# Performance work log

Hardware: AMD Instinct MI355X
Metric: run time of the kernel (lower is better)

## Reference

```python
import jax, jax.numpy as jnp
import numpy as np

B = 4096          # batch; ALSO the QLSTM sequence length (forward unbinds dim 0)
IN_DIM = 8
HIDDEN = 16       # hidden_dim == n_qubits (required for torch broadcast to work)
TAGSET = 10

_H = jnp.array([[1, 1], [1, -1]], jnp.complex64) * (2.0 ** -0.5)

# ---- single/two-qubit gate builders (qiskit conventions) ----

def _rz(t):
    t = jnp.asarray(t, jnp.float32)
    em = jnp.exp(-0.5j * t)
    ep = jnp.exp(0.5j * t)
    z = jnp.zeros((), jnp.complex64)
    return jnp.stack([jnp.stack([em, z]), jnp.stack([z, ep])])

def _ry(t):
    t = jnp.asarray(t, jnp.float32)
    c = jnp.cos(0.5 * t).astype(jnp.complex64)
    s = jnp.sin(0.5 * t).astype(jnp.complex64)
    return jnp.stack([jnp.stack([c, -s]), jnp.stack([s, c])])

def _phase(lam):  # qiskit p / u1 gate: diag(1, e^{i*lam})
    lam = jnp.asarray(lam, jnp.float32)
    one = jnp.ones((), jnp.complex64)
    z = jnp.zeros((), jnp.complex64)
    return jnp.stack([jnp.stack([one, z]), jnp.stack([z, jnp.exp(1j * lam)])])

# ---- statevector primitives: state has shape (2,)*n, axis i == qubit i ----

def _apply1(state, gate, w):
    s = jnp.tensordot(gate, state, axes=([1], [w]))
    return jnp.moveaxis(s, 0, w)

def _cnot(state, c, t):
    s = jnp.moveaxis(state, (c, t), (0, 1))
    s = jnp.stack([s[0], s[1][::-1]], axis=0)  # flip target where control==1
    return jnp.moveaxis(s, (0, 1), (c, t))

def _expZ(state, w):
    p = state.real ** 2 + state.imag ** 2
    p = jnp.moveaxis(p, w, 0).reshape(2, -1).sum(axis=1)
    return p[0] - p[1]

def _conv(state, a, b, p):
    state = _apply1(state, _rz(-np.pi / 2), b)
    state = _cnot(state, b, a)
    state = _apply1(state, _rz(p[0]), a)
    state = _apply1(state, _ry(p[1]), b)
    state = _cnot(state, a, b)
    state = _apply1(state, _ry(p[2]), b)
    state = _cnot(state, b, a)
    state = _apply1(state, _rz(np.pi / 2), a)
    return state

def _pool(state, a, b, p):
    state = _apply1(state, _rz(-np.pi / 2), b)
    state = _cnot(state, b, a)
    state = _apply1(state, _rz(p[0]), a)
    state = _apply1(state, _ry(p[1]), b)
    state = _cnot(state, a, b)
    state = _apply1(state, _ry(p[2]), b)
    return state

def _qcnn_one(x, c1, p1, c2, p2, c3, p3):
    state = jnp.zeros((2,) * 8, jnp.complex64).at[(0,) * 8].set(1.0)
    for _ in range(2):  # ZFeatureMap(8), reps=2: H layer + P(2*x_i)
        for q in range(8):
            state = _apply1(state, _H, q)
        for q in range(8):
            state = _apply1(state, _phase(2.0 * x[q]), q)
    for k, i in enumerate(range(0, 8, 2)):   # c1 on pairs (0,1)(2,3)(4,5)(6,7)
        state = _conv(state, i, i + 1, c1[k])
    for k in range(4):                        # p1 on (0,4)(1,5)(2,6)(3,7)
        state = _pool(state, k, k + 4, p1[k])
    for k, i in enumerate(range(0, 4, 2)):   # c2 on (0,1)(2,3)
        state = _conv(state, i, i + 1, c2[k])
    for k in range(2):                        # p2 on (0,2)(1,3)
        state = _pool(state, k, k + 2, p2[k])
    state = _conv(state, 0, 1, c3[0])
    state = _pool(state, 0, 1, p3[0])
    return _expZ(state, 7)  # observable 'Z'+'I'*7 == Z on qubit 7

def _sampler_one(x, w):
    state = jnp.zeros((2, 2), jnp.complex64).at[0, 0].set(1.0)
    state = _apply1(state, _ry(x[0]), 0)
    state = _apply1(state, _ry(x[1]), 1)
    state = _cnot(state, 0, 1)
    state = _apply1(state, _ry(w[0]), 0)
    state = _apply1(state, _ry(w[1]), 1)
    state = _cnot(state, 0, 1)
    state = _apply1(state, _ry(w[2]), 0)
    state = _apply1(state, _ry(w[3]), 1)
    probs = state.real ** 2 + state.imag ** 2  # [q0, q1]
    return probs.T.reshape(4)  # qiskit little-endian: index = 2*q1 + q0

# ---- QLSTM QLayer, exact closed form ----
# product state RX(v_i + theta_i)|0>, CNOT ring (0,1)..(n-2,n-1),(n-1,0), <Z_j>:
#   <Z_0> = prod_{k>=1} cos(phi_k);  <Z_j> = prod_{k<=j} cos(phi_k) for j>=1.

def _qlayer(v, theta):  # v: [1, n]
    c = jnp.cos(v + theta)
    head = jnp.prod(c[:, 1:], axis=1, keepdims=True)
    rest = jnp.cumprod(c, axis=1)[:, 1:]
    return jnp.concatenate([head, rest], axis=1)

def _forward(inputs, c1, p1, c2, p2, c3, p3, w_smp, Wf, bf, Wi, bi, Wu, bu, Wo, bo, th_f, th_i, th_u, th_o, Wt, bt):
    qcnn = jax.vmap(lambda x: _qcnn_one(x, c1, p1, c2, p2, c3, p3))(inputs)[:, None]  # [B,1]
    samp = jax.vmap(lambda x: _sampler_one(x, w_smp))(inputs)  # [B,4]
    seq = inputs[:, None, :]  # [T=B, 1, 8] -- unsqueeze(1) then unbind(dim=0)

    def step(carry, x):
        hx, cx = carry
        comb = jnp.concatenate([x, hx], axis=1)  # [1, 24]
        f = jax.nn.sigmoid(_qlayer(comb @ Wf.T + bf, th_f))
        i = jax.nn.sigmoid(_qlayer(comb @ Wi.T + bi, th_i))
        g = jnp.tanh(_qlayer(comb @ Wu.T + bu, th_u))
        o = jax.nn.sigmoid(_qlayer(comb @ Wo.T + bo, th_o))
        cx = f * cx + i * g
        hx = o * jnp.tanh(cx)
        return (hx, cx), hx

    z0 = jnp.zeros((1, HIDDEN), jnp.float32)
    _, outs = jax.lax.scan(step, (z0, z0), seq)  # [B, 1, 16]
    tag = jax.nn.log_softmax(outs @ Wt.T + bt, axis=-1)  # [B, 1, 10]
    return qcnn, tag, samp

def setup_inputs() -> dict:
    key = jax.random.key(0)
    ks = jax.random.split(key, 32)
    pi = float(np.pi)
    u = lambda k, s: jax.random.uniform(k, s, jnp.float32, -pi, pi)
    fan = IN_DIM + HIDDEN
    lw = lambda k: jax.random.normal(k, (HIDDEN, fan), jnp.float32) * fan ** -0.5
    lb = lambda k: jax.random.normal(k, (HIDDEN,), jnp.float32) * fan ** -0.5
    return {
        "inputs": jax.random.normal(ks[0], (B, IN_DIM), jnp.float32),
        "c1": u(ks[1], (4, 3)), "p1": u(ks[2], (4, 3)),
        "c2": u(ks[3], (2, 3)), "p2": u(ks[4], (2, 3)),
        "c3": u(ks[5], (1, 3)), "p3": u(ks[6], (1, 3)),
        "w_smp": u(ks[7], (4,)),
        "Wf": lw(ks[8]), "bf": lb(ks[9]),
        "Wi": lw(ks[10]), "bi": lb(ks[11]),
        "Wu": lw(ks[12]), "bu": lb(ks[13]),
        "Wo": lw(ks[14]), "bo": lb(ks[15]),
        "th_f": u(ks[16], (HIDDEN,)), "th_i": u(ks[17], (HIDDEN,)),
        "th_u": u(ks[18], (HIDDEN,)), "th_o": u(ks[19], (HIDDEN,)),
        "Wt": jax.random.normal(ks[20], (TAGSET, HIDDEN), jnp.float32) * HIDDEN ** -0.5,
        "bt": jax.random.normal(ks[21], (TAGSET,), jnp.float32) * HIDDEN ** -0.5,
    }

def reference(inputs, c1, p1, c2, p2, c3, p3, w_smp, Wf, bf, Wi, bi, Wu, bu, Wo, bo, th_f, th_i, th_u, th_o, Wt, bt):
    return _forward(inputs, c1, p1, c2, p2, c3, p3, w_smp, Wf, bf, Wi, bi, Wu, bu, Wo, bo, th_f, th_i, th_u, th_o, Wt, bt)
```

## Files before the change

### kernel.cpp

```cpp
#include <hip/hip_runtime.h>
#include <math.h>


typedef unsigned int uint32x2 __attribute__((ext_vector_type(2)));

#define INV2PI 0.15915494309189535f
#define NCHUNK 128
#define CHUNK  32
#define WARM   96
#define MAXSTEP (CHUNK + WARM)

__device__ __forceinline__ float2 cmulf(float2 a, float2 b){
  return make_float2(a.x*b.x - a.y*b.y, a.x*b.y + a.y*b.x);
}
template<int CTRL>
__device__ __forceinline__ float dpp_mov(float v){
  return __int_as_float(__builtin_amdgcn_update_dpp(
      0, __float_as_int(v), CTRL, 0xF, 0xF, false));
}

#define PFX_LEVEL(p, CTRLSTR) \
  asm("v_mul_f32_dpp %0, %0, %0 " CTRLSTR " row_mask:0xf bank_mask:0xf" : "+v"(p))
#define FMAC_DPP(acc, src, w, CTRLSTR) \
  asm("v_fmac_f32_dpp %0, %1, %2 " CTRLSTR " row_mask:0xf bank_mask:0xf" \
      : "+v"(acc) : "v"(src), "v"(w))

struct SerState {
  float wh[16];
  float esc, gA, gB;
  int   e;
  bool  c32, c16, b0, b1, mQ;
};

__device__ __forceinline__ void lstm_step(const SerState& S, float ax,
                                          float& cx, float& h){
  const float r0  = h;
  const float r4  = dpp_mov<0x124>(r0);
  const float r8  = dpp_mov<0x128>(r0);
  const float r12 = dpp_mov<0x12C>(r0);
  float a0 = fmaf(S.wh[0],  r0,  ax);
  float a1 = S.wh[4]  * r4;
  float a2 = S.wh[8]  * r8;
  float a3 = S.wh[12] * r12;
  FMAC_DPP(a0, r0,  S.wh[1],  "row_ror:1");
  FMAC_DPP(a1, r4,  S.wh[5],  "row_ror:1");
  FMAC_DPP(a2, r8,  S.wh[9],  "row_ror:1");
  FMAC_DPP(a3, r12, S.wh[13], "row_ror:1");
  FMAC_DPP(a0, r0,  S.wh[2],  "row_ror:2");
  FMAC_DPP(a1, r4,  S.wh[6],  "row_ror:2");
  FMAC_DPP(a2, r8,  S.wh[10], "row_ror:2");
  FMAC_DPP(a3, r12, S.wh[14], "row_ror:2");
  FMAC_DPP(a0, r0,  S.wh[3],  "row_ror:3");
  FMAC_DPP(a1, r4,  S.wh[7],  "row_ror:3");
  FMAC_DPP(a2, r8,  S.wh[11], "row_ror:3");
  FMAC_DPP(a3, r12, S.wh[15], "row_ror:3");
  const float acc = (a0+a1) + (a2+a3);

  const float c = __builtin_amdgcn_cosf(acc);
  float p = c;
  float sfx = (S.e==0) ? 1.0f : c;
  PFX_LEVEL(p,   "row_shr:1");
  PFX_LEVEL(sfx, "row_shl:1");
  PFX_LEVEL(p,   "row_shr:2");
  PFX_LEVEL(sfx, "row_shl:2");
  PFX_LEVEL(p,   "row_shr:4");
  PFX_LEVEL(sfx, "row_shl:4");
  PFX_LEVEL(p,   "row_shr:8");
  PFX_LEVEL(sfx, "row_shl:8");
  const float v = (S.e==0) ? sfx : p;

  const float ex  = __builtin_amdgcn_exp2f(v * S.esc);
  const float sg  = __builtin_amdgcn_rcpf(1.0f + ex);
  const float act = fmaf(S.gA, sg, S.gB);

  const unsigned au = __float_as_uint(act);
  uint32x2 r32 = __builtin_amdgcn_permlane32_swap(au, au, false, false);
  const unsigned o32u = S.c32 ? r32[0] : r32[1];
  uint32x2 rA = __builtin_amdgcn_permlane16_swap(au, au, false, false);
  const unsigned oAu = S.c16 ? rA[0] : rA[1];
  uint32x2 rB = __builtin_amdgcn_permlane16_swap(o32u, o32u, false, false);
  const unsigned oBu = S.c16 ? rB[0] : rB[1];
  const float fau = __uint_as_float(au);
  const float fA  = __uint_as_float(oAu);
  const float f32 = __uint_as_float(o32u);
  const float fB  = __uint_as_float(oBu);
  const float pLoA = S.b0 ? fA  : fau;
  const float pHiA = S.b0 ? fB  : f32;
  const float act0 = S.b1 ? pHiA : pLoA;
  const float pLoB = S.b0 ? fau : fA;
  const float pHiB = S.b0 ? f32 : fB;
  const float act3 = S.b1 ? pLoB : pHiB;
  const float Q    = S.mQ ? fA*f32 : fau*fB;

  cx = fmaf(act0, cx, Q);
  const float em = __builtin_amdgcn_exp2f(cx * -2.885390082f);
  const float rr = __builtin_amdgcn_rcpf(1.0f + em);
  h = fmaf(act3+act3, rr, -act3);
}

__device__ __forceinline__ void ser_init(SerState& S, int lane,
    const float* Wf, const float* Wi, const float* Wu, const float* Wo){
  const int g = lane >> 4, e = lane & 15;
  S.e = e;
  const float* W = (g==0)?Wf:(g==1)?Wi:(g==2)?Wu:Wo;
  int probe = __builtin_amdgcn_update_dpp(0, e, 0x121, 0xF, 0xF, false);
  const int sgn = (probe == ((e+1)&15)) ? 1 : -1;
  #pragma unroll
  for (int d=0; d<16; d++)
    S.wh[d] = W[e*24 + 8 + ((e + sgn*d + 32) & 15)] * INV2PI;
  S.esc = (g==2) ? -2.885390082f : -1.442695041f;
  S.gA  = (g==2) ? 2.0f : 1.0f;
  S.gB  = (g==2) ? -1.0f : 0.0f;
  uint32x2 p32 = __builtin_amdgcn_permlane32_swap((unsigned)lane,(unsigned)lane,false,false);
  S.c32 = (p32[0] == (unsigned)(lane ^ 32));
  uint32x2 p16 = __builtin_amdgcn_permlane16_swap((unsigned)lane,(unsigned)lane,false,false);
  S.c16 = (p16[0] == (unsigned)(lane ^ 16));
  S.b0 = (g & 1) != 0;
  S.b1 = (g & 2) != 0;
  S.mQ = (g==0) || (g==3);
}

__device__ __forceinline__ void apply_diag(float2 (&s)[4], int q, float2 d0, float2 d1){
  const int lane = threadIdx.x & 63;
  #pragma unroll
  for (int r=0;r<4;r++){
    int bit = (q>=6) ? ((r >> (7-q)) & 1) : ((lane >> (5-q)) & 1);
    s[r] = cmulf(s[r], bit ? d1 : d0);
  }
}
__device__ __forceinline__ void apply_real(float2 (&s)[4], int q,
                                           float m00, float m01, float m10, float m11){
  const int lane = threadIdx.x & 63;
  if (q >= 6){
    const int st = 1 << (7-q);
    for (int base=0;base<4;base++){
      if (base & st) continue;
      float2 a = s[base], b2 = s[base+st];
      s[base]    = make_float2(fmaf(m00,a.x, m01*b2.x), fmaf(m00,a.y, m01*b2.y));
      s[base+st] = make_float2(fmaf(m10,a.x, m11*b2.x), fmaf(m10,a.y, m11*b2.y));
    }
  } else {
    const int mask = 1 << (5-q);
    const bool hi = (lane & mask) != 0;
    #pragma unroll
    for (int r=0;r<4;r++){
      float ox = __shfl_xor(s[r].x, mask);
      float oy = __shfl_xor(s[r].y, mask);
      float2 m = s[r];
      if (!hi) s[r] = make_float2(fmaf(m00,m.x, m01*ox), fmaf(m00,m.y, m01*oy));
      else     s[r] = make_float2(fmaf(m10,ox, m11*m.x), fmaf(m10,oy, m11*m.y));
    }
  }
}
__device__ __forceinline__ void cnot_g(float2 (&s)[4], int c, int t){
  const int lane = threadIdx.x & 63;
  if (t >= 6){
    const int st = 1 << (7-t);
    for (int base=0;base<4;base++){
      if (base & st) continue;
      int cb = (c>=6) ? ((base >> (7-c)) & 1) : ((lane >> (5-c)) & 1);
      if (cb){ float2 tmp=s[base]; s[base]=s[base+st]; s[base+st]=tmp; }
    }
  } else {
    const int mask = 1 << (5-t);
    #pragma unroll
    for (int r=0;r<4;r++){
      float ox = __shfl_xor(s[r].x, mask);
      float oy = __shfl_xor(s[r].y, mask);
      int cb = (c>=6) ? ((r >> (7-c)) & 1) : ((lane >> (5-c)) & 1);
      if (cb) s[r] = make_float2(ox, oy);
    }
  }
}
__device__ void conv_g(float2 (&s)[4], int qa, int qb, const float* p){
  const float R = 0.70710678118654752f;
  apply_diag(s, qb, make_float2(R,R), make_float2(R,-R));
  cnot_g(s, qb, qa);
  float sn, cs;
  __sincosf(0.5f*p[0], &sn, &cs);
  apply_diag(s, qa, make_float2(cs,-sn), make_float2(cs,sn));
  __sincosf(0.5f*p[1], &sn, &cs);
  apply_real(s, qb, cs, -sn, sn, cs);
  cnot_g(s, qa, qb);
  __sincosf(0.5f*p[2], &sn, &cs);
  apply_real(s, qb, cs, -sn, sn, cs);
  cnot_g(s, qb, qa);
  apply_diag(s, qa, make_float2(R,-R), make_float2(R,R));
}
__device__ void pool_g(float2 (&s)[4], int qa, int qb, const float* p){
  const float R = 0.70710678118654752f;
  apply_diag(s, qb, make_float2(R,R), make_float2(R,-R));
  cnot_g(s, qb, qa);
  float sn, cs;
  __sincosf(0.5f*p[0], &sn, &cs);
  apply_diag(s, qa, make_float2(cs,-sn), make_float2(cs,sn));
  __sincosf(0.5f*p[1], &sn, &cs);
  apply_real(s, qb, cs, -sn, sn, cs);
  cnot_g(s, qa, qb);
  __sincosf(0.5f*p[2], &sn, &cs);
  apply_real(s, qb, cs, -sn, sn, cs);
}

__device__ void qcnn_body(const float* __restrict__ inputs,
                          const float* __restrict__ c1, const float* __restrict__ p1,
                          const float* __restrict__ c2, const float* __restrict__ p2,
                          const float* __restrict__ c3, const float* __restrict__ p3,
                          const float* __restrict__ w_smp,
                          float* __restrict__ out, int b, int B)
{
  const int lane = threadIdx.x & 63;
  float2 s[4];
  s[0] = make_float2(0.f,0.f); s[1]=s[0]; s[2]=s[0]; s[3]=s[0];
  if (lane == 0) s[0] = make_float2(1.f, 0.f);
  float xl[8];
  #pragma unroll
  for (int k=0;k<8;k++) xl[k] = inputs[b*8+k];
  const float R = 0.70710678118654752f;
  for (int rep=0;rep<2;rep++){
    for (int q=0;q<8;q++) apply_real(s, q, R, R, R, -R);
    for (int q=0;q<8;q++){
      float sn, cs; __sincosf(2.0f*xl[q], &sn, &cs);
      apply_diag(s, q, make_float2(1.f,0.f), make_float2(cs,sn));
    }
  }
  for (int k=0;k<4;k++) conv_g(s, 2*k, 2*k+1, c1+3*k);
  for (int k=0;k<4;k++) pool_g(s, k, k+4, p1+3*k);
  for (int k=0;k<2;k++) conv_g(s, 2*k, 2*k+1, c2+3*k);
  for (int k=0;k<2;k++) pool_g(s, k, k+2, p2+3*k);
  conv_g(s, 0, 1, c3);
  pool_g(s, 0, 1, p3);
  float v = (s[0].x*s[0].x + s[0].y*s[0].y) - (s[1].x*s[1].x + s[1].y*s[1].y)
          + (s[2].x*s[2].x + s[2].y*s[2].y) - (s[3].x*s[3].x + s[3].y*s[3].y);
  #pragma unroll
  for (int d=1; d<64; d<<=1) v += __shfl_xor(v, d);
  if (lane == 0){
    out[b] = v;
    float a00=1.f, a01=0.f, a10=0.f, a11=0.f;
    float sn, cs, t0, t1;
    #define RY0(T) { __sincosf(0.5f*(T), &sn, &cs); \
      t0 = cs*a00 - sn*a10; t1 = sn*a00 + cs*a10; a00=t0; a10=t1; \
      t0 = cs*a01 - sn*a11; t1 = sn*a01 + cs*a11; a01=t0; a11=t1; }
    #define RY1(T) { __sincosf(0.5f*(T), &sn, &cs); \
      t0 = cs*a00 - sn*a01; t1 = sn*a00 + cs*a01; a00=t0; a01=t1; \
      t0 = cs*a10 - sn*a11; t1 = sn*a10 + cs*a11; a10=t0; a11=t1; }
    #define CN01 { float tmp=a10; a10=a11; a11=tmp; }
    RY0(xl[0]); RY1(xl[1]); CN01;
    RY0(w_smp[0]); RY1(w_smp[1]); CN01;
    RY0(w_smp[2]); RY1(w_smp[3]);
    #undef RY0
    #undef RY1
    #undef CN01
    float* samp = out + B + B*10;
    samp[b*4+0] = a00*a00; samp[b*4+1] = a10*a10;
    samp[b*4+2] = a01*a01; samp[b*4+3] = a11*a11;
  }
}

extern "C" __global__ void __launch_bounds__(256)
k_all(const float* __restrict__ inputs,
      const float* __restrict__ Wf, const float* __restrict__ Wi,
      const float* __restrict__ Wu, const float* __restrict__ Wo,
      const float* __restrict__ bfv, const float* __restrict__ biv,
      const float* __restrict__ buv, const float* __restrict__ bov,
      const float* __restrict__ thf, const float* __restrict__ thi,
      const float* __restrict__ thu, const float* __restrict__ tho,
      const float* __restrict__ c1, const float* __restrict__ p1,
      const float* __restrict__ c2, const float* __restrict__ p2,
      const float* __restrict__ c3, const float* __restrict__ p3,
      const float* __restrict__ w_smp,
      const float* __restrict__ Wt, const float* __restrict__ bt,
      float* __restrict__ out, int B)
{
  __shared__ float xlds[MAXSTEP*8];
  __shared__ float hlds[16*CHUNK];

  if (blockIdx.x < NCHUNK){
    const int kc    = blockIdx.x;
    const int t_out = kc*CHUNK, t_end = t_out + CHUNK;
    const int t_start = (t_out > WARM) ? (t_out - WARM) : 0;
    const int nsteps  = t_end - t_start;

    for (int i = threadIdx.x; i < nsteps*8; i += 256)
      xlds[i] = inputs[t_start*8 + i];
    __syncthreads();

    if (threadIdx.x < 64){
      const int lane = threadIdx.x, g = lane>>4, e = lane&15;
      SerState S; ser_init(S, lane, Wf, Wi, Wu, Wo);
      const float* W  = (g==0)?Wf :(g==1)?Wi :(g==2)?Wu :Wo;
      const float* bb = (g==0)?bfv:(g==1)?biv:(g==2)?buv:bov;
      const float* th = (g==0)?thf:(g==1)?thi:(g==2)?thu:tho;
      float wx[8];
      #pragma unroll
      for (int k2=0;k2<8;k2++) wx[k2] = W[e*24+k2] * INV2PI;
      const float base = (bb[e] + th[e]) * INV2PI;

      float cx=0.f, h=0.f, hq0=0.f, hq1=0.f, hq2=0.f;
      float4 xa = *(const float4*)&xlds[0];
      float4 xb = *(const float4*)&xlds[4];
      float u0 = fmaf(wx[0],xa.x,base), u1 = wx[1]*xa.y,
            u2 = wx[2]*xa.z,            u3 = wx[3]*xa.w;
      u0 = fmaf(wx[4],xb.x,u0); u1 = fmaf(wx[5],xb.y,u1);
      u2 = fmaf(wx[6],xb.z,u2); u3 = fmaf(wx[7],xb.w,u3);
      float axc = (u0+u1)+(u2+u3);

      #pragma unroll 4
      for (int lt=0; lt<nsteps; lt++){
        const int nlt = (lt+1 < nsteps) ? (lt+1) : lt;
        const float4 na = *(const float4*)&xlds[nlt*8];
        const float4 nb = *(const float4*)&xlds[nlt*8+4];
        float v0 = fmaf(wx[0],na.x,base), v1 = wx[1]*na.y,
              v2 = wx[2]*na.z,            v3 = wx[3]*na.w;
        v0 = fmaf(wx[4],nb.x,v0); v1 = fmaf(wx[5],nb.y,v1);
        v2 = fmaf(wx[6],nb.z,v2); v3 = fmaf(wx[7],nb.w,v3);
        const float axn = (v0+v1)+(v2+v3);

        lstm_step(S, axc, cx, h);
        const int q = lt & 3;
        if      (q==0) hq0 = h;
        else if (q==1) hq1 = h;
        else if (q==2) hq2 = h;
        else {
          const int tb = t_start + lt - 3;
          if (tb >= t_out){
            const float hv = S.b1 ? (S.b0 ? h : hq2) : (S.b0 ? hq1 : hq0);
            hlds[e*CHUNK + (tb + g - t_out)] = hv;
          }
        }
        axc = axn;
      }
    }
    __syncthreads();

    if (threadIdx.x < CHUNK){
      const int s = threadIdx.x;
      float hh[16];
      #pragma unroll
      for (int e2=0;e2<16;e2++) hh[e2] = hlds[e2*CHUNK + s];
      float lg[10];
      #pragma unroll
      for (int j=0;j<10;j++){
        const float* w = Wt + j*16;
        float s0 = fmaf(w[0],hh[0], bt[j]);
        float s1 = w[1]*hh[1], s2 = w[2]*hh[2], s3 = w[3]*hh[3];
        #pragma unroll
        for (int e2=4;e2<16;e2+=4){
          s0 = fmaf(w[e2],  hh[e2],  s0);
          s1 = fmaf(w[e2+1],hh[e2+1],s1);
          s2 = fmaf(w[e2+2],hh[e2+2],s2);
          s3 = fmaf(w[e2+3],hh[e2+3],s3);
        }
        lg[j] = (s0+s1)+(s2+s3);
      }
      float m = lg[0];
      #pragma unroll
      for (int j=1;j<10;j++) m = fmaxf(m, lg[j]);
      float ss = 0.f;
      #pragma unroll
      for (int j=0;j<10;j++) ss += __expf(lg[j]-m);
      const float lse = __logf(ss) + m;
      float* tag = out + B + (size_t)(t_out + s)*10;
      #pragma unroll
      for (int j=0;j<10;j++) tag[j] = lg[j] - lse;
    }
    return;
  }

  const int b = (blockIdx.x - NCHUNK)*4 + (threadIdx.x >> 6);
  qcnn_body(inputs, c1,p1,c2,p2,c3,p3, w_smp, out, b, B);
}

extern "C" void kernel_launch(void* const* d_in, const int* in_sizes, int n_in,
                              void* d_out, int out_size, void* d_ws, size_t ws_size,
                              hipStream_t stream)
{
  const float* inputs = (const float*)d_in[0];
  const float* c1  = (const float*)d_in[1];
  const float* p1  = (const float*)d_in[2];
  const float* c2  = (const float*)d_in[3];
  const float* p2  = (const float*)d_in[4];
  const float* c3  = (const float*)d_in[5];
  const float* p3  = (const float*)d_in[6];
  const float* wsm = (const float*)d_in[7];
  const float* Wf  = (const float*)d_in[8];
  const float* bf_ = (const float*)d_in[9];
  const float* Wi  = (const float*)d_in[10];
  const float* bi_ = (const float*)d_in[11];
  const float* Wu  = (const float*)d_in[12];
  const float* bu_ = (const float*)d_in[13];
  const float* Wo  = (const float*)d_in[14];
  const float* bo_ = (const float*)d_in[15];
  const float* thf = (const float*)d_in[16];
  const float* thi = (const float*)d_in[17];
  const float* thu = (const float*)d_in[18];
  const float* tho = (const float*)d_in[19];
  const float* Wt  = (const float*)d_in[20];
  const float* bt  = (const float*)d_in[21];
  const int B = in_sizes[0] / 8;
  float* out = (float*)d_out;

  k_all<<<NCHUNK + B/4, 256, 0, stream>>>(inputs,
                                          Wf,Wi,Wu,Wo, bf_,bi_,bu_,bo_,
                                          thf,thi,thu,tho,
                                          c1,p1,c2,p2,c3,p3, wsm,
                                          Wt, bt, out, B);
}
```

Before: 133.5 us.

## Reduce QCNN to measured-qubit light cone, one thread per sample

```diff
diff --git a/kernel.cpp b/kernel.cpp
--- a/kernel.cpp
+++ b/kernel.cpp
@@ -9,6 +9,7 @@
 #define CHUNK  32
 #define WARM   96
 #define MAXSTEP (CHUNK + WARM)
+#define HLDS_LD (CHUNK + 1)
 
 __device__ __forceinline__ float2 cmulf(float2 a, float2 b){
   return make_float2(a.x*b.x - a.y*b.y, a.x*b.y + a.y*b.x);
@@ -120,140 +121,118 @@
   S.mQ = (g==0) || (g==3);
 }
 
-__device__ __forceinline__ void apply_diag(float2 (&s)[4], int q, float2 d0, float2 d1){
-  const int lane = threadIdx.x & 63;
+__device__ __forceinline__ void rz4_lo(float2 (&t)[4], float sn, float cs){
+  const float2 e0 = make_float2(cs,-sn), e1 = make_float2(cs, sn);
+  t[0]=cmulf(t[0],e0); t[1]=cmulf(t[1],e1);
+  t[2]=cmulf(t[2],e0); t[3]=cmulf(t[3],e1);
+}
+__device__ __forceinline__ void rz4_hi(float2 (&t)[4], float sn, float cs){
+  const float2 e0 = make_float2(cs,-sn), e1 = make_float2(cs, sn);
+  t[0]=cmulf(t[0],e0); t[1]=cmulf(t[1],e0);
+  t[2]=cmulf(t[2],e1); t[3]=cmulf(t[3],e1);
+}
+__device__ __forceinline__ void ry4_lo(float2 (&t)[4], float sn, float cs){
+  float2 a=t[0], b=t[1];
+  t[0]=make_float2(cs*a.x - sn*b.x, cs*a.y - sn*b.y);
+  t[1]=make_float2(sn*a.x + cs*b.x, sn*a.y + cs*b.y);
+  a=t[2]; b=t[3];
+  t[2]=make_float2(cs*a.x - sn*b.x, cs*a.y - sn*b.y);
+  t[3]=make_float2(sn*a.x + cs*b.x, sn*a.y + cs*b.y);
+}
+__device__ __forceinline__ void cnot4_loctl(float2 (&t)[4]){
+  float2 tmp=t[1]; t[1]=t[3]; t[3]=tmp;
+}
+__device__ __forceinline__ void cnot4_hictl(float2 (&t)[4]){
+  float2 tmp=t[2]; t[2]=t[3]; t[3]=tmp;
+}
+
+__device__ __forceinline__ void conv4(float2 (&t)[4], const float* p){
+  const float R = 0.70710678118654752f;
+  rz4_lo(t, -R, R);
+  cnot4_loctl(t);
+  float sn, cs;
+  __sincosf(0.5f*p[0], &sn, &cs);
+  rz4_hi(t, sn, cs);
+  __sincosf(0.5f*p[1], &sn, &cs);
+  ry4_lo(t, sn, cs);
+  cnot4_hictl(t);
+  __sincosf(0.5f*p[2], &sn, &cs);
+  ry4_lo(t, sn, cs);
+  cnot4_loctl(t);
+  rz4_hi(t, R, R);
+}
+__device__ __forceinline__ void pool4(float2 (&t)[4], const float* p){
+  const float R = 0.70710678118654752f;
+  rz4_lo(t, -R, R);
+  cnot4_loctl(t);
+  float sn, cs;
+  __sincosf(0.5f*p[0], &sn, &cs);
+  rz4_hi(t, sn, cs);
+  __sincosf(0.5f*p[1], &sn, &cs);
+  ry4_lo(t, sn, cs);
+  cnot4_hictl(t);
+  __sincosf(0.5f*p[2], &sn, &cs);
+  ry4_lo(t, sn, cs);
+}
+
+__device__ void qcnn_thread(const float* __restrict__ inputs,
+                            const float* __restrict__ c1,
+                            const float* __restrict__ p1,
+                            const float* __restrict__ w_smp,
+                            float* __restrict__ out, int b, int B)
+{
+  const float4 xa = *(const float4*)(inputs + b*8);
+  const float4 xb = *(const float4*)(inputs + b*8 + 4);
+
+  const float xs[4] = {xa.z, xa.w, xb.z, xb.w};
+  float2 v0[4], v1[4];
   #pragma unroll
-  for (int r=0;r<4;r++){
-    int bit = (q>=6) ? ((r >> (7-q)) & 1) : ((lane >> (5-q)) & 1);
-    s[r] = cmulf(s[r], bit ? d1 : d0);
+  for (int k=0;k<4;k++){
+    float sn, cs; __sincosf(2.0f*xs[k], &sn, &cs);
+    v0[k] = make_float2(0.5f*(1.0f+cs), 0.5f*sn);
+    v1[k] = make_float2(0.5f*(cs - cs*cs + sn*sn), 0.5f*(sn - 2.0f*cs*sn));
   }
-}
-__device__ __forceinline__ void apply_real(float2 (&s)[4], int q,
-                                           float m00, float m01, float m10, float m11){
-  const int lane = threadIdx.x & 63;
-  if (q >= 6){
-    const int st = 1 << (7-q);
-    for (int base=0;base<4;base++){
-      if (base & st) continue;
-      float2 a = s[base], b2 = s[base+st];
-      s[base]    = make_float2(fmaf(m00,a.x, m01*b2.x), fmaf(m00,a.y, m01*b2.y));
-      s[base+st] = make_float2(fmaf(m10,a.x, m11*b2.x), fmaf(m10,a.y, m11*b2.y));
-    }
-  } else {
-    const int mask = 1 << (5-q);
-    const bool hi = (lane & mask) != 0;
+  float2 A[4]  = {cmulf(v0[0],v0[1]), cmulf(v0[0],v1[1]),
+                  cmulf(v1[0],v0[1]), cmulf(v1[0],v1[1])};
+  float2 Bv[4] = {cmulf(v0[2],v0[3]), cmulf(v0[2],v1[3]),
+                  cmulf(v1[2],v0[3]), cmulf(v1[2],v1[3])};
+  conv4(A,  c1+3);
+  conv4(Bv, c1+9);
+
+  float ez = 0.f;
+  #pragma unroll
+  for (int i2=0;i2<2;i2++){
     #pragma unroll
-    for (int r=0;r<4;r++){
-      float ox = __shfl_xor(s[r].x, mask);
-      float oy = __shfl_xor(s[r].y, mask);
-      float2 m = s[r];
-      if (!hi) s[r] = make_float2(fmaf(m00,m.x, m01*ox), fmaf(m00,m.y, m01*oy));
-      else     s[r] = make_float2(fmaf(m10,ox, m11*m.x), fmaf(m10,oy, m11*m.y));
+    for (int i6=0;i6<2;i6++){
+      float2 t[4] = {cmulf(A[i2*2+0], Bv[i6*2+0]),
+                     cmulf(A[i2*2+0], Bv[i6*2+1]),
+                     cmulf(A[i2*2+1], Bv[i6*2+0]),
+                     cmulf(A[i2*2+1], Bv[i6*2+1])};
+      pool4(t, p1+9);
+      ez += (t[0].x*t[0].x + t[0].y*t[0].y) - (t[1].x*t[1].x + t[1].y*t[1].y)
+          + (t[2].x*t[2].x + t[2].y*t[2].y) - (t[3].x*t[3].x + t[3].y*t[3].y);
     }
   }
-}
-__device__ __forceinline__ void cnot_g(float2 (&s)[4], int c, int t){
-  const int lane = threadIdx.x & 63;
-  if (t >= 6){
-    const int st = 1 << (7-t);
-    for (int base=0;base<4;base++){
-      if (base & st) continue;
-      int cb = (c>=6) ? ((base >> (7-c)) & 1) : ((lane >> (5-c)) & 1);
-      if (cb){ float2 tmp=s[base]; s[base]=s[base+st]; s[base+st]=tmp; }
-    }
-  } else {
-    const int mask = 1 << (5-t);
-    #pragma unroll
-    for (int r=0;r<4;r++){
-      float ox = __shfl_xor(s[r].x, mask);
-      float oy = __shfl_xor(s[r].y, mask);
-      int cb = (c>=6) ? ((r >> (7-c)) & 1) : ((lane >> (5-c)) & 1);
-      if (cb) s[r] = make_float2(ox, oy);
-    }
-  }
-}
-__device__ void conv_g(float2 (&s)[4], int qa, int qb, const float* p){
-  const float R = 0.70710678118654752f;
-  apply_diag(s, qb, make_float2(R,R), make_float2(R,-R));
-  cnot_g(s, qb, qa);
-  float sn, cs;
-  __sincosf(0.5f*p[0], &sn, &cs);
-  apply_diag(s, qa, make_float2(cs,-sn), make_float2(cs,sn));
-  __sincosf(0.5f*p[1], &sn, &cs);
-  apply_real(s, qb, cs, -sn, sn, cs);
-  cnot_g(s, qa, qb);
-  __sincosf(0.5f*p[2], &sn, &cs);
-  apply_real(s, qb, cs, -sn, sn, cs);
-  cnot_g(s, qb, qa);
-  apply_diag(s, qa, make_float2(R,-R), make_float2(R,R));
-}
-__device__ void pool_g(float2 (&s)[4], int qa, int qb, const float* p){
-  const float R = 0.70710678118654752f;
-  apply_diag(s, qb, make_float2(R,R), make_float2(R,-R));
-  cnot_g(s, qb, qa);
-  float sn, cs;
-  __sincosf(0.5f*p[0], &sn, &cs);
-  apply_diag(s, qa, make_float2(cs,-sn), make_float2(cs,sn));
-  __sincosf(0.5f*p[1], &sn, &cs);
-  apply_real(s, qb, cs, -sn, sn, cs);
-  cnot_g(s, qa, qb);
-  __sincosf(0.5f*p[2], &sn, &cs);
-  apply_real(s, qb, cs, -sn, sn, cs);
-}
-
-__device__ void qcnn_body(const float* __restrict__ inputs,
-                          const float* __restrict__ c1, const float* __restrict__ p1,
-                          const float* __restrict__ c2, const float* __restrict__ p2,
-                          const float* __restrict__ c3, const float* __restrict__ p3,
-                          const float* __restrict__ w_smp,
-                          float* __restrict__ out, int b, int B)
-{
-  const int lane = threadIdx.x & 63;
-  float2 s[4];
-  s[0] = make_float2(0.f,0.f); s[1]=s[0]; s[2]=s[0]; s[3]=s[0];
-  if (lane == 0) s[0] = make_float2(1.f, 0.f);
-  float xl[8];
-  #pragma unroll
-  for (int k=0;k<8;k++) xl[k] = inputs[b*8+k];
-  const float R = 0.70710678118654752f;
-  for (int rep=0;rep<2;rep++){
-    for (int q=0;q<8;q++) apply_real(s, q, R, R, R, -R);
-    for (int q=0;q<8;q++){
-      float sn, cs; __sincosf(2.0f*xl[q], &sn, &cs);
-      apply_diag(s, q, make_float2(1.f,0.f), make_float2(cs,sn));
-    }
-  }
-  for (int k=0;k<4;k++) conv_g(s, 2*k, 2*k+1, c1+3*k);
-  for (int k=0;k<4;k++) pool_g(s, k, k+4, p1+3*k);
-  for (int k=0;k<2;k++) conv_g(s, 2*k, 2*k+1, c2+3*k);
-  for (int k=0;k<2;k++) pool_g(s, k, k+2, p2+3*k);
-  conv_g(s, 0, 1, c3);
-  pool_g(s, 0, 1, p3);
-  float v = (s[0].x*s[0].x + s[0].y*s[0].y) - (s[1].x*s[1].x + s[1].y*s[1].y)
-          + (s[2].x*s[2].x + s[2].y*s[2].y) - (s[3].x*s[3].x + s[3].y*s[3].y);
-  #pragma unroll
-  for (int d=1; d<64; d<<=1) v += __shfl_xor(v, d);
-  if (lane == 0){
-    out[b] = v;
-    float a00=1.f, a01=0.f, a10=0.f, a11=0.f;
-    float sn, cs, t0, t1;
-    #define RY0(T) { __sincosf(0.5f*(T), &sn, &cs); \
-      t0 = cs*a00 - sn*a10; t1 = sn*a00 + cs*a10; a00=t0; a10=t1; \
-      t0 = cs*a01 - sn*a11; t1 = sn*a01 + cs*a11; a01=t0; a11=t1; }
-    #define RY1(T) { __sincosf(0.5f*(T), &sn, &cs); \
-      t0 = cs*a00 - sn*a01; t1 = sn*a00 + cs*a01; a00=t0; a01=t1; \
-      t0 = cs*a10 - sn*a11; t1 = sn*a10 + cs*a11; a10=t0; a11=t1; }
-    #define CN01 { float tmp=a10; a10=a11; a11=tmp; }
-    RY0(xl[0]); RY1(xl[1]); CN01;
-    RY0(w_smp[0]); RY1(w_smp[1]); CN01;
-    RY0(w_smp[2]); RY1(w_smp[3]);
-    #undef RY0
-    #undef RY1
-    #undef CN01
-    float* samp = out + B + B*10;
-    samp[b*4+0] = a00*a00; samp[b*4+1] = a10*a10;
-    samp[b*4+2] = a01*a01; samp[b*4+3] = a11*a11;
-  }
+  out[b] = ez;
+
+  float a00=1.f, a01=0.f, a10=0.f, a11=0.f;
+  float sn, cs, t0, t1;
+  #define RY0(T) { __sincosf(0.5f*(T), &sn, &cs); \
+    t0 = cs*a00 - sn*a10; t1 = sn*a00 + cs*a10; a00=t0; a10=t1; \
+    t0 = cs*a01 - sn*a11; t1 = sn*a01 + cs*a11; a01=t0; a11=t1; }
+  #define RY1(T) { __sincosf(0.5f*(T), &sn, &cs); \
+    t0 = cs*a00 - sn*a01; t1 = sn*a00 + cs*a01; a00=t0; a01=t1; \
+    t0 = cs*a10 - sn*a11; t1 = sn*a10 + cs*a11; a10=t0; a11=t1; }
+  #define CN01 { float tmp=a10; a10=a11; a11=tmp; }
+  RY0(xa.x); RY1(xa.y); CN01;
+  RY0(w_smp[0]); RY1(w_smp[1]); CN01;
+  RY0(w_smp[2]); RY1(w_smp[3]);
+  #undef RY0
+  #undef RY1
+  #undef CN01
+  float* samp = out + B + B*10;
+  samp[b*4+0] = a00*a00; samp[b*4+1] = a10*a10;
+  samp[b*4+2] = a01*a01; samp[b*4+3] = a11*a11;
 }
 
 extern "C" __global__ void __launch_bounds__(256)
@@ -265,14 +244,12 @@
       const float* __restrict__ thf, const float* __restrict__ thi,
       const float* __restrict__ thu, const float* __restrict__ tho,
       const float* __restrict__ c1, const float* __restrict__ p1,
-      const float* __restrict__ c2, const float* __restrict__ p2,
-      const float* __restrict__ c3, const float* __restrict__ p3,
       const float* __restrict__ w_smp,
       const float* __restrict__ Wt, const float* __restrict__ bt,
       float* __restrict__ out, int B)
 {
   __shared__ float xlds[MAXSTEP*8];
-  __shared__ float hlds[16*CHUNK];
+  __shared__ float hlds[16*HLDS_LD];
 
   if (blockIdx.x < NCHUNK){
     const int kc    = blockIdx.x;
@@ -296,12 +273,12 @@
       const float base = (bb[e] + th[e]) * INV2PI;
 
       float cx=0.f, h=0.f, hq0=0.f, hq1=0.f, hq2=0.f;
-      float4 xa = *(const float4*)&xlds[0];
-      float4 xb = *(const float4*)&xlds[4];
-      float u0 = fmaf(wx[0],xa.x,base), u1 = wx[1]*xa.y,
-            u2 = wx[2]*xa.z,            u3 = wx[3]*xa.w;
-      u0 = fmaf(wx[4],xb.x,u0); u1 = fmaf(wx[5],xb.y,u1);
-      u2 = fmaf(wx[6],xb.z,u2); u3 = fmaf(wx[7],xb.w,u3);
+      float4 za = *(const float4*)&xlds[0];
+      float4 zb = *(const float4*)&xlds[4];
+      float u0 = fmaf(wx[0],za.x,base), u1 = wx[1]*za.y,
+            u2 = wx[2]*za.z,            u3 = wx[3]*za.w;
+      u0 = fmaf(wx[4],zb.x,u0); u1 = fmaf(wx[5],zb.y,u1);
+      u2 = fmaf(wx[6],zb.z,u2); u3 = fmaf(wx[7],zb.w,u3);
       float axc = (u0+u1)+(u2+u3);
 
       #pragma unroll 4
@@ -324,7 +301,7 @@
           const int tb = t_start + lt - 3;
           if (tb >= t_out){
             const float hv = S.b1 ? (S.b0 ? h : hq2) : (S.b0 ? hq1 : hq0);
-            hlds[e*CHUNK + (tb + g - t_out)] = hv;
+            hlds[e*HLDS_LD + (tb + g - t_out)] = hv;
           }
         }
         axc = axn;
@@ -336,7 +313,7 @@
       const int s = threadIdx.x;
       float hh[16];
       #pragma unroll
-      for (int e2=0;e2<16;e2++) hh[e2] = hlds[e2*CHUNK + s];
+      for (int e2=0;e2<16;e2++) hh[e2] = hlds[e2*HLDS_LD + s];
       float lg[10];
       #pragma unroll
       for (int j=0;j<10;j++){
@@ -366,8 +343,8 @@
     return;
   }
 
-  const int b = (blockIdx.x - NCHUNK)*4 + (threadIdx.x >> 6);
-  qcnn_body(inputs, c1,p1,c2,p2,c3,p3, w_smp, out, b, B);
+  const int b = (blockIdx.x - NCHUNK)*256 + threadIdx.x;
+  if (b < B) qcnn_thread(inputs, c1, p1, w_smp, out, b, B);
 }
 
 extern "C" void kernel_launch(void* const* d_in, const int* in_sizes, int n_in,
@@ -377,10 +354,6 @@
   const float* inputs = (const float*)d_in[0];
   const float* c1  = (const float*)d_in[1];
   const float* p1  = (const float*)d_in[2];
-  const float* c2  = (const float*)d_in[3];
-  const float* p2  = (const float*)d_in[4];
-  const float* c3  = (const float*)d_in[5];
-  const float* p3  = (const float*)d_in[6];
   const float* wsm = (const float*)d_in[7];
   const float* Wf  = (const float*)d_in[8];
   const float* bf_ = (const float*)d_in[9];
@@ -399,9 +372,9 @@
   const int B = in_sizes[0] / 8;
   float* out = (float*)d_out;
 
-  k_all<<<NCHUNK + B/4, 256, 0, stream>>>(inputs,
+  k_all<<<NCHUNK + (B+255)/256, 256, 0, stream>>>(inputs,
                                           Wf,Wi,Wu,Wo, bf_,bi_,bu_,bo_,
                                           thf,thi,thu,tho,
-                                          c1,p1,c2,p2,c3,p3, wsm,
+                                          c1, p1, wsm,
                                           Wt, bt, out, B);
 }
```

Result: faster. 124.5 us (-6.7%).
